# Performance work log

Measured on AMD Instinct MI355X. Metric: run time of the kernel, lower is better.

## Reference

```python
import jax, jax.numpy as jnp
import numpy as np

H = 16          # num_attention_heads
D = 1024        # input_size == hidden_size
HD = D // H     # attention_head_size = 64
EPS = 1e-12


def setup_inputs() -> dict:
    key = jax.random.key(0)
    ks = jax.random.split(key, 12)
    B, S = 4, 2048
    sc = 1.0 / np.sqrt(D)
    return {
        "x": jax.random.normal(ks[0], (B, S, D), jnp.float32),
        "y": jax.random.normal(ks[1], (B, S, D), jnp.float32),
        "Wq": jax.random.normal(ks[2], (D, D), jnp.float32) * sc,
        "bq": jnp.zeros((D,), jnp.float32),
        "Wk": jax.random.normal(ks[3], (D, D), jnp.float32) * sc,
        "bk": jnp.zeros((D,), jnp.float32),
        "Wv": jax.random.normal(ks[4], (D, D), jnp.float32) * sc,
        "bv": jnp.zeros((D,), jnp.float32),
        "Wd": jax.random.normal(ks[5], (D, D), jnp.float32) * sc,
        "bd": jnp.zeros((D,), jnp.float32),
        "gamma": jnp.ones((D,), jnp.float32),
        "beta": jnp.zeros((D,), jnp.float32),
        "debug": 0,
    }


def _split_heads(t):
    B, S, _ = t.shape
    return t.reshape(B, S, H, HD).transpose(0, 2, 1, 3)  # [B,H,S,hd]


def reference(x, y, Wq, bq, Wk, bk, Wv, bv, Wd, bd, gamma, beta, debug):
    # torch Linear: t @ W.T + b
    q = _split_heads(x @ Wq.T + bq)   # query from x
    k = _split_heads(y @ Wk.T + bk)   # key from y
    v = _split_heads(x @ Wv.T + bv)   # value from x (as in source)
    scores = jnp.einsum("bhqd,bhkd->bhqk", q, k) / np.sqrt(HD)
    probs = jax.nn.softmax(scores, axis=-1)  # dropout: eval mode (identity)
    ctx = jnp.einsum("bhqk,bhkd->bhqd", probs, v)
    B, _, S, _ = ctx.shape
    ctx = ctx.transpose(0, 2, 1, 3).reshape(B, S, D)
    h = ctx @ Wd.T + bd               # out_dropout: eval mode (identity)
    h = h + x
    u = h.mean(-1, keepdims=True)
    s = jnp.square(h - u).mean(-1, keepdims=True)
    h = (h - u) / jnp.sqrt(s + EPS)
    return gamma * h + beta
```

## Files before the change

### kernel.cpp

```cpp
#include <hip/hip_runtime.h>
#include <hip/hip_bf16.h>
#include <stdint.h>


typedef unsigned short ushortT;
typedef __attribute__((ext_vector_type(8))) __bf16 bf16x8;
typedef __attribute__((ext_vector_type(4))) float f32x4;
typedef __attribute__((ext_vector_type(16))) float f32x16;
typedef __attribute__((ext_vector_type(8))) unsigned short ushort8;
typedef __attribute__((ext_vector_type(4))) unsigned short ushort4v;

__device__ __forceinline__ unsigned short f2bf(float f) {
  union { float f; unsigned u; } x; x.f = f;
  unsigned r = (x.u + 0x7FFFu + ((x.u >> 16) & 1u)) >> 16;
  return (unsigned short)r;
}

__device__ __forceinline__ unsigned cvtpk_bf16(float lo, float hi) {
  unsigned r;
  asm("v_cvt_pk_bf16_f32 %0, %1, %2" : "=v"(r) : "v"(lo), "v"(hi));
  return r;
}

__device__ __forceinline__ void load_lds16(const void* g, void* l) {
  __builtin_amdgcn_global_load_lds(
      (const __attribute__((address_space(1))) void*)g,
      (__attribute__((address_space(3))) void*)l, 16, 0, 0);
}

__device__ __forceinline__ f32x4 mfma16(bf16x8 a, bf16x8 b, f32x4 c) {
  return __builtin_amdgcn_mfma_f32_16x16x32_bf16(a, b, c, 0, 0, 0);
}
__device__ __forceinline__ f32x16 mfma32(bf16x8 a, bf16x8 b, f32x16 c) {
  return __builtin_amdgcn_mfma_f32_32x32x16_bf16(a, b, c, 0, 0, 0);
}

__global__ __launch_bounds__(256) void k_cvt2(const float* __restrict__ a,
                                              const float* __restrict__ b,
                                              ushortT* __restrict__ oa,
                                              ushortT* __restrict__ ob) {
  const float* in = blockIdx.z ? b : a;
  ushortT* out = blockIdx.z ? ob : oa;
  int i = blockIdx.x * 256 + threadIdx.x;
  const float4* p = (const float4*)in;
  float4 u = p[(size_t)i * 2];
  float4 v = p[(size_t)i * 2 + 1];
  ushort8 o;
  o[0] = f2bf(u.x); o[1] = f2bf(u.y); o[2] = f2bf(u.z); o[3] = f2bf(u.w);
  o[4] = f2bf(v.x); o[5] = f2bf(v.y); o[6] = f2bf(v.z); o[7] = f2bf(v.w);
  *(ushort8*)(out + (size_t)i * 8) = o;
}

__global__ __launch_bounds__(256) void k_cvtw(const float* __restrict__ w0,
                                              const float* __restrict__ w1,
                                              const float* __restrict__ w2,
                                              const float* __restrict__ w3,
                                              ushortT* __restrict__ o0,
                                              ushortT* __restrict__ o1,
                                              ushortT* __restrict__ o2,
                                              ushortT* __restrict__ o3) {
  int z = blockIdx.z;
  const float* in = (z == 0) ? w0 : (z == 1) ? w1 : (z == 2) ? w2 : w3;
  ushortT* out = (z == 0) ? o0 : (z == 1) ? o1 : (z == 2) ? o2 : o3;
  int i = blockIdx.x * 256 + threadIdx.x;
  const float4* p = (const float4*)in;
  float4 u = p[(size_t)i * 2];
  float4 v = p[(size_t)i * 2 + 1];
  ushort8 o;
  o[0] = f2bf(u.x); o[1] = f2bf(u.y); o[2] = f2bf(u.z); o[3] = f2bf(u.w);
  o[4] = f2bf(v.x); o[5] = f2bf(v.y); o[6] = f2bf(v.z); o[7] = f2bf(v.w);
  *(ushort8*)(out + (size_t)i * 8) = o;
}

__global__ __launch_bounds__(256, 2) void k_gemm(
    const ushortT* __restrict__ xbf, const ushortT* __restrict__ ybf,
    const ushortT* __restrict__ wq, const ushortT* __restrict__ wk,
    const ushortT* __restrict__ wv, const ushortT* __restrict__ wd,
    const float* __restrict__ bq, const float* __restrict__ bk,
    const float* __restrict__ bv, const float* __restrict__ bd,
    const ushortT* __restrict__ ctx, const float* __restrict__ xres,
    ushortT* __restrict__ Qo, ushortT* __restrict__ Ko,
    ushortT* __restrict__ Vt, float* __restrict__ Ho, int mode_base) {
  __shared__ ushortT lA[2][128 * 64];
  __shared__ ushortT lB[2][128 * 64];
  const int t = threadIdx.x;
  const int lane = t & 63;
  const int w = t >> 6;
  const int wm = w >> 1, wn = w & 1;
  const int mode = mode_base + blockIdx.z;
  const int flat = blockIdx.x + (blockIdx.y << 3);
  const int xcd = flat & 7, j = flat >> 3;
  const int m0 = (xcd * 8 + (j >> 3)) * 128;
  const int n0 = (j & 7) * 128;

  const ushortT* A = (mode == 1) ? ybf : (mode == 3 ? ctx : xbf);
  const ushortT* W = (mode == 0) ? wq : (mode == 1 ? wk : (mode == 2 ? wv : wd));
  const float* bias = (mode == 0) ? bq : (mode == 1 ? bk : (mode == 2 ? bv : bd));

  f32x4 z = {0.f, 0.f, 0.f, 0.f};
  f32x4 acc[4][4];
#pragma unroll
  for (int i = 0; i < 4; ++i)
#pragma unroll
    for (int j2 = 0; j2 < 4; ++j2) acc[i][j2] = z;

  const int so = t * 16;
  const int srow = so >> 7;
  const int skb = (so & 127) ^ ((srow & 7) << 4);
  const ushortT* asrc = A + (size_t)(m0 + srow) * 1024 + (skb >> 1);
  const ushortT* wsrc = W + (size_t)(n0 + srow) * 1024 + (skb >> 1);

#define GSTAGE(buf, k0)                                                     \
  do {                                                                      \
    _Pragma("unroll")                                                       \
    for (int c = 0; c < 4; ++c) {                                           \
      load_lds16(asrc + (k0) + (size_t)c * 32 * 1024,                       \
                 (char*)&lA[buf][0] + c * 4096 + t * 16);                   \
      load_lds16(wsrc + (k0) + (size_t)c * 32 * 1024,                       \
                 (char*)&lB[buf][0] + c * 4096 + t * 16);                   \
    }                                                                       \
  } while (0)

  GSTAGE(0, 0);
  __syncthreads();
  int cur = 0;
  for (int k0 = 0; k0 < 1024; k0 += 64) {
    if (k0 + 64 < 1024) GSTAGE(cur ^ 1, k0 + 64);
#pragma unroll
    for (int kk = 0; kk < 2; ++kk) {
      bf16x8 af[4], bfr[4];
#pragma unroll
      for (int i = 0; i < 4; ++i) {
        int arow = wm * 64 + i * 16 + (lane & 15);
        int ak = ((kk * 32 + (lane >> 4) * 8) * 2) ^ ((arow & 7) << 4);
        af[i] = *(const bf16x8*)((const char*)&lA[cur][0] + arow * 128 + ak);
        int brow = wn * 64 + i * 16 + (lane & 15);
        int bk2 = ((kk * 32 + (lane >> 4) * 8) * 2) ^ ((brow & 7) << 4);
        bfr[i] = *(const bf16x8*)((const char*)&lB[cur][0] + brow * 128 + bk2);
      }
      __builtin_amdgcn_s_setprio(1);
#pragma unroll
      for (int i = 0; i < 4; ++i)
#pragma unroll
        for (int j2 = 0; j2 < 4; ++j2)
          acc[i][j2] = mfma16(af[i], bfr[j2], acc[i][j2]);
      __builtin_amdgcn_s_setprio(0);
    }
    __syncthreads();
    cur ^= 1;
  }
#undef GSTAGE

  const int cm = wm * 64 + (lane >> 4) * 4;
  const int cn = wn * 64 + (lane & 15);
  if (mode == 3) {
#pragma unroll
    for (int mi = 0; mi < 4; ++mi)
#pragma unroll
      for (int ni = 0; ni < 4; ++ni) {
        int n = n0 + cn + ni * 16;
        float bn = bias[n];
#pragma unroll
        for (int r = 0; r < 4; ++r) {
          int m = m0 + cm + mi * 16 + r;
          Ho[(size_t)m * 1024 + n] =
              acc[mi][ni][r] + bn + xres[(size_t)m * 1024 + n];
        }
      }
  } else if (mode == 2) {
#pragma unroll
    for (int mi = 0; mi < 4; ++mi)
#pragma unroll
      for (int ni = 0; ni < 4; ++ni) {
        int n = n0 + cn + ni * 16;
        int hh = n >> 6, hd = n & 63;
        float bn = bias[n];
        int m_ = m0 + cm + mi * 16;
        int b = m_ >> 11, s = m_ & 2047;
        ushort4v pk;
#pragma unroll
        for (int r = 0; r < 4; ++r) pk[r] = f2bf(acc[mi][ni][r] + bn);
        *(ushort4v*)&Vt[(((size_t)(b * 16 + hh) * 64 + hd) << 11) + s] = pk;
      }
  } else {
    ushortT* O = (mode == 0) ? Qo : Ko;
    const float qs = (mode == 0) ? 0.18033688011112042f : 1.0f;
#pragma unroll
    for (int mi = 0; mi < 4; ++mi)
#pragma unroll
      for (int ni = 0; ni < 4; ++ni) {
        int n = n0 + cn + ni * 16;
        int hh = n >> 6, hd = n & 63;
        float bn = bias[n];
#pragma unroll
        for (int r = 0; r < 4; ++r) {
          int m = m0 + cm + mi * 16 + r;
          int b = m >> 11, s = m & 2047;
          O[(((size_t)(b * 16 + hh) * 2048 + s) << 6) + hd] =
              f2bf((acc[mi][ni][r] + bn) * qs);
        }
      }
  }
}

__global__ __launch_bounds__(256, 4) void k_attn(const ushortT* __restrict__ Q,
                                                 const ushortT* __restrict__ K,
                                                 const ushortT* __restrict__ Vt,
                                                 ushortT* __restrict__ ctx) {
  __shared__ ushortT lK[2][4096];
  __shared__ ushortT lV[2][4096];
  const int t = threadIdx.x, lane = t & 63, w = t >> 6;
  const int hi = lane >> 5, l31 = lane & 31;
  const int i0 = blockIdx.x;
  const int xcd = i0 & 7, j0 = i0 >> 3;
  const int bh = xcd * 8 + (j0 >> 4);
  const int qt = j0 & 15;
  const int q0 = qt * 128 + w * 32;

  const ushortT* Qb = Q + ((size_t)bh * 2048 + q0) * 64;
  const ushortT* Kb = K + (size_t)bh * 2048 * 64;
  const ushortT* Vb = Vt + (size_t)bh * 64 * 2048;

  bf16x8 qf[4];
#pragma unroll
  for (int dc = 0; dc < 4; ++dc)
    qf[dc] = *(const bf16x8*)(Qb + l31 * 64 + dc * 16 + hi * 8);

  union { unsigned short us[8]; bf16x8 v; } ones_u;
#pragma unroll
  for (int i = 0; i < 8; ++i) ones_u.us[i] = 0x3F80;

  f32x16 accO0, accO1, accL;
#pragma unroll
  for (int i = 0; i < 16; ++i) { accO0[i] = 0.f; accO1[i] = 0.f; accL[i] = 0.f; }

  const int srow = t >> 3;
  const int scolb = ((t & 7) * 16) ^ ((srow & 7) << 4);
  const ushortT* ksrc = Kb + srow * 64 + (scolb >> 1);
  const ushortT* vsrc = Vb + (size_t)srow * 2048 + (scolb >> 1);
  const int swz = (lane & 7) << 4;
  const int hs = (hi * 16) ^ swz;
  const int krowb = l31 * 128;

#define STAGE(buf, kk)                                                        \
  do {                                                                        \
    load_lds16(ksrc + (size_t)(kk) * 64, (char*)&lK[buf][0] + w * 1024);      \
    load_lds16(ksrc + 2048 + (size_t)(kk) * 64,                               \
               (char*)&lK[buf][0] + 4096 + w * 1024);                         \
    load_lds16(vsrc + (kk), (char*)&lV[buf][0] + w * 1024);                   \
    load_lds16(vsrc + 65536 + (kk), (char*)&lV[buf][0] + 4096 + w * 1024);    \
  } while (0)

  STAGE(0, 0);
  __syncthreads();
  int cur = 0;
  for (int k0 = 0; k0 < 2048; k0 += 64) {
    if (k0 + 64 < 2048) STAGE(cur ^ 1, k0 + 64);
    const char* lKc = (const char*)&lK[cur][0];
    const char* lVc = (const char*)&lV[cur][0];
#pragma unroll
    for (int kb = 0; kb < 2; ++kb) {
      f32x16 sc;
#pragma unroll
      for (int i = 0; i < 16; ++i) sc[i] = 0.f;
      __builtin_amdgcn_s_setprio(1);
#pragma unroll
      for (int dc = 0; dc < 4; ++dc) {
        bf16x8 kf = *(const bf16x8*)(lKc + kb * 4096 + krowb + ((dc * 32) ^ hs));
        sc = mfma32(kf, qf[dc], sc);
      }
      __builtin_amdgcn_s_setprio(0);
      float p[16];
#pragma unroll
      for (int r = 0; r < 16; ++r) p[r] = __builtin_amdgcn_exp2f(sc[r]);
      union { unsigned u[4]; bf16x8 v; } pa0, pa1;
#pragma unroll
      for (int i = 0; i < 4; ++i) {
        int base = (i >> 1) * 8 + (i & 1) * 2;
        unsigned a = cvtpk_bf16(p[base], p[base + 1]);
        unsigned b = cvtpk_bf16(p[base + 4], p[base + 5]);
        asm("v_permlane32_swap_b32 %0, %1" : "+v"(a), "+v"(b));
        if (i >> 1) { pa1.u[i & 1] = a; pa1.u[2 + (i & 1)] = b; }
        else        { pa0.u[i & 1] = a; pa0.u[2 + (i & 1)] = b; }
      }
      __builtin_amdgcn_s_setprio(1);
#pragma unroll
      for (int nb = 0; nb < 2; ++nb) {
        const char* vrow = lVc + (nb * 32 + l31) * 128;
        bf16x8 vf0 = *(const bf16x8*)(vrow + ((kb * 64) ^ hs));
        bf16x8 vf1 = *(const bf16x8*)(vrow + ((kb * 64 + 32) ^ hs));
        f32x16& ao = nb ? accO1 : accO0;
        ao = mfma32(pa0.v, vf0, ao);
        ao = mfma32(pa1.v, vf1, ao);
      }
      accL = mfma32(pa0.v, ones_u.v, accL);
      accL = mfma32(pa1.v, ones_u.v, accL);
      __builtin_amdgcn_s_setprio(0);
    }
    __syncthreads();
    cur ^= 1;
  }
#undef STAGE

  int b = bh >> 4, hh = bh & 15;
  ushortT* cb = ctx + ((size_t)(b * 2048 + q0)) * 1024 + hh * 64;
#pragma unroll
  for (int r = 0; r < 16; ++r) {
    int qm = (r & 3) + 8 * (r >> 2) + 4 * hi;
    float lr = 1.0f / accL[r];
    size_t rb = (size_t)qm * 1024;
    cb[rb + l31] = f2bf(accO0[r] * lr);
    cb[rb + 32 + l31] = f2bf(accO1[r] * lr);
  }
}

__global__ __launch_bounds__(256) void k_ln(const float* __restrict__ Hi,
                                            const float* __restrict__ gamma,
                                            const float* __restrict__ beta,
                                            float* __restrict__ out) {
  const int row = blockIdx.x, t = threadIdx.x, lane = t & 63, w = t >> 6;
  const float4* hp = (const float4*)(Hi + (size_t)row * 1024);
  float4 v = hp[t];
  float s1 = v.x + v.y + v.z + v.w;
  float s2 = v.x * v.x + v.y * v.y + v.z * v.z + v.w * v.w;
#pragma unroll
  for (int off = 1; off < 64; off <<= 1) {
    s1 += __shfl_xor(s1, off);
    s2 += __shfl_xor(s2, off);
  }
  __shared__ float red[8];
  if (lane == 0) { red[w] = s1; red[4 + w] = s2; }
  __syncthreads();
  s1 = red[0] + red[1] + red[2] + red[3];
  s2 = red[4] + red[5] + red[6] + red[7];
  float u = s1 * (1.f / 1024.f);
  float var = s2 * (1.f / 1024.f) - u * u;
  float rstd = rsqrtf(var + 1e-12f);
  float4 g = ((const float4*)gamma)[t];
  float4 bb = ((const float4*)beta)[t];
  float4 oo;
  oo.x = (v.x - u) * rstd * g.x + bb.x;
  oo.y = (v.y - u) * rstd * g.y + bb.y;
  oo.z = (v.z - u) * rstd * g.z + bb.z;
  oo.w = (v.w - u) * rstd * g.w + bb.w;
  ((float4*)(out + (size_t)row * 1024))[t] = oo;
}

extern "C" void kernel_launch(void* const* d_in, const int* in_sizes, int n_in,
                              void* d_out, int out_size, void* d_ws,
                              size_t ws_size, hipStream_t stream) {
  const float* x = (const float*)d_in[0];
  const float* y = (const float*)d_in[1];
  const float* Wq = (const float*)d_in[2];
  const float* bq = (const float*)d_in[3];
  const float* Wk = (const float*)d_in[4];
  const float* bk = (const float*)d_in[5];
  const float* Wv = (const float*)d_in[6];
  const float* bv = (const float*)d_in[7];
  const float* Wd = (const float*)d_in[8];
  const float* bd = (const float*)d_in[9];
  const float* gamma = (const float*)d_in[10];
  const float* beta = (const float*)d_in[11];

  char* ws = (char*)d_ws;
  ushortT* xbf = (ushortT*)(ws + 0);
  ushortT* ybf = (ushortT*)(ws + 16777216);
  ushortT* wqb = (ushortT*)(ws + 33554432);
  ushortT* wkb = (ushortT*)(ws + 35651584);
  ushortT* wvb = (ushortT*)(ws + 37748736);
  ushortT* wdb = (ushortT*)(ws + 39845888);
  ushortT* Qb = (ushortT*)(ws + 41943040);
  ushortT* Kb = (ushortT*)(ws + 58720256);
  ushortT* Vtb = (ushortT*)(ws + 75497472);
  ushortT* ctx = (ushortT*)(ws + 92274688);
  float* Hbuf = (float*)(ws + 0);

  k_cvt2<<<dim3(4096, 1, 2), 256, 0, stream>>>(x, y, xbf, ybf);
  k_cvtw<<<dim3(512, 1, 4), 256, 0, stream>>>(Wq, Wk, Wv, Wd, wqb, wkb, wvb,
                                              wdb);

  k_gemm<<<dim3(8, 64, 3), 256, 0, stream>>>(xbf, ybf, wqb, wkb, wvb, wdb, bq,
                                             bk, bv, bd, ctx, x, Qb, Kb, Vtb,
                                             Hbuf, 0);
  k_attn<<<1024, 256, 0, stream>>>(Qb, Kb, Vtb, ctx);
  k_gemm<<<dim3(8, 64, 1), 256, 0, stream>>>(xbf, ybf, wqb, wkb, wvb, wdb, bq,
                                             bk, bv, bd, ctx, x, Qb, Kb, Vtb,
                                             Hbuf, 3);
  k_ln<<<8192, 256, 0, stream>>>(Hbuf, gamma, beta, (float*)d_out);
}
```

Before: 196.5 us.

## Prefetch two GEMM k-stages ahead with vmcnt waits and merge conversion kernels

The GEMM main loop now issues loads two stages ahead into the double buffer. It waits with a partial s_waitcnt vmcnt so the next stage's loads stay in flight while the current stage computes, and reissues the load into the just-consumed buffer after a barrier. This is meant to hide global-to-LDS latency better than the previous one-stage-ahead scheme with a full syncthreads. The two fp32-to-bf16 conversion kernels are also merged into one launch to save launch overhead. The hand-counted vmcnt value relies on exactly 8 outstanding loads per stage, so it is fragile if the stage's load count changes.

```diff
diff --git a/kernel.cpp b/kernel.cpp
--- a/kernel.cpp
+++ b/kernel.cpp
@@ -35,34 +35,28 @@
   return __builtin_amdgcn_mfma_f32_32x32x16_bf16(a, b, c, 0, 0, 0);
 }
 
-__global__ __launch_bounds__(256) void k_cvt2(const float* __restrict__ a,
-                                              const float* __restrict__ b,
-                                              ushortT* __restrict__ oa,
-                                              ushortT* __restrict__ ob) {
-  const float* in = blockIdx.z ? b : a;
-  ushortT* out = blockIdx.z ? ob : oa;
-  int i = blockIdx.x * 256 + threadIdx.x;
-  const float4* p = (const float4*)in;
-  float4 u = p[(size_t)i * 2];
-  float4 v = p[(size_t)i * 2 + 1];
-  ushort8 o;
-  o[0] = f2bf(u.x); o[1] = f2bf(u.y); o[2] = f2bf(u.z); o[3] = f2bf(u.w);
-  o[4] = f2bf(v.x); o[5] = f2bf(v.y); o[6] = f2bf(v.z); o[7] = f2bf(v.w);
-  *(ushort8*)(out + (size_t)i * 8) = o;
-}
-
-__global__ __launch_bounds__(256) void k_cvtw(const float* __restrict__ w0,
-                                              const float* __restrict__ w1,
-                                              const float* __restrict__ w2,
-                                              const float* __restrict__ w3,
-                                              ushortT* __restrict__ o0,
-                                              ushortT* __restrict__ o1,
-                                              ushortT* __restrict__ o2,
-                                              ushortT* __restrict__ o3) {
-  int z = blockIdx.z;
-  const float* in = (z == 0) ? w0 : (z == 1) ? w1 : (z == 2) ? w2 : w3;
-  ushortT* out = (z == 0) ? o0 : (z == 1) ? o1 : (z == 2) ? o2 : o3;
-  int i = blockIdx.x * 256 + threadIdx.x;
+__global__ __launch_bounds__(256) void k_cvt_all(
+    const float* __restrict__ x, const float* __restrict__ y,
+    const float* __restrict__ w0, const float* __restrict__ w1,
+    const float* __restrict__ w2, const float* __restrict__ w3,
+    ushortT* __restrict__ ox, ushortT* __restrict__ oy,
+    ushortT* __restrict__ o0, ushortT* __restrict__ o1,
+    ushortT* __restrict__ o2, ushortT* __restrict__ o3) {
+  int b = blockIdx.x;
+  const float* in;
+  ushortT* out;
+  int blk;
+  if (b < 4096) {
+    in = x; out = ox; blk = b;
+  } else if (b < 8192) {
+    in = y; out = oy; blk = b - 4096;
+  } else {
+    int z = (b - 8192) >> 9;
+    blk = (b - 8192) & 511;
+    in = (z == 0) ? w0 : (z == 1) ? w1 : (z == 2) ? w2 : w3;
+    out = (z == 0) ? o0 : (z == 1) ? o1 : (z == 2) ? o2 : o3;
+  }
+  int i = blk * 256 + threadIdx.x;
   const float4* p = (const float4*)in;
   float4 u = p[(size_t)i * 2];
   float4 v = p[(size_t)i * 2 + 1];
@@ -122,10 +116,17 @@
   } while (0)
 
   GSTAGE(0, 0);
-  __syncthreads();
+  GSTAGE(1, 64);
   int cur = 0;
   for (int k0 = 0; k0 < 1024; k0 += 64) {
-    if (k0 + 64 < 1024) GSTAGE(cur ^ 1, k0 + 64);
+    if (k0 < 960) {
+      asm volatile("s_waitcnt vmcnt(8)" ::: "memory");
+    } else {
+      asm volatile("s_waitcnt vmcnt(0)" ::: "memory");
+    }
+    __builtin_amdgcn_sched_barrier(0);
+    __builtin_amdgcn_s_barrier();
+    __builtin_amdgcn_sched_barrier(0);
 #pragma unroll
     for (int kk = 0; kk < 2; ++kk) {
       bf16x8 af[4], bfr[4];
@@ -146,7 +147,10 @@
           acc[i][j2] = mfma16(af[i], bfr[j2], acc[i][j2]);
       __builtin_amdgcn_s_setprio(0);
     }
-    __syncthreads();
+    __builtin_amdgcn_sched_barrier(0);
+    __builtin_amdgcn_s_barrier();
+    __builtin_amdgcn_sched_barrier(0);
+    if (k0 + 128 < 1024) GSTAGE(cur, k0 + 128);
     cur ^= 1;
   }
 #undef GSTAGE
@@ -375,9 +379,8 @@
   ushortT* ctx = (ushortT*)(ws + 92274688);
   float* Hbuf = (float*)(ws + 0);
 
-  k_cvt2<<<dim3(4096, 1, 2), 256, 0, stream>>>(x, y, xbf, ybf);
-  k_cvtw<<<dim3(512, 1, 4), 256, 0, stream>>>(Wq, Wk, Wv, Wd, wqb, wkb, wvb,
-                                              wdb);
+  k_cvt_all<<<10240, 256, 0, stream>>>(x, y, Wq, Wk, Wv, Wd, xbf, ybf, wqb,
+                                       wkb, wvb, wdb);
 
   k_gemm<<<dim3(8, 64, 3), 256, 0, stream>>>(xbf, ybf, wqb, wkb, wvb, wdb, bq,
                                              bk, bv, bd, ctx, x, Qb, Kb, Vtb,
```

After: 200.8 us. +2.2%, slower.
